# Kernel optimization log

Measured on AMD Instinct MI355X. Metric: run time of the kernel, lower is better.

Reference implementation:

```python
import jax, jax.numpy as jnp
import numpy as np

N_NODES = 100000
N_REL = 4
N_EDGES = 160000  # per relation
IN_F, HID_F, OUT_F = 128, 128, 64


def hetero_layer(x, edges, W, b):
    """Sum over relations of GraphConv (norm='both'): D_in^-1/2 A_r D_out^-1/2 X W_r + b_r."""
    N = x.shape[0]
    out = jnp.zeros((N, W.shape[2]), dtype=x.dtype)
    for r in range(W.shape[0]):  # small fixed relation count
        src = edges[r, 0]
        dst = edges[r, 1]
        ones = jnp.ones(src.shape[0], dtype=x.dtype)
        deg_out = jnp.clip(jax.ops.segment_sum(ones, src, num_segments=N), 1.0)
        deg_in = jnp.clip(jax.ops.segment_sum(ones, dst, num_segments=N), 1.0)
        # scale src features, project (W first since in_feats >= out_feats), gather, scatter-sum
        h = (x * jax.lax.rsqrt(deg_out)[:, None]) @ W[r]
        agg = jax.ops.segment_sum(h[src], dst, num_segments=N)
        out = out + agg * jax.lax.rsqrt(deg_in)[:, None] + b[r]
    return out


def setup_inputs() -> dict:
    key = jax.random.key(0)
    ks = jax.random.split(key, 6)
    x = jax.random.normal(ks[0], (N_NODES, IN_F), dtype=jnp.float32)
    edges = jax.random.randint(ks[1], (N_REL, 2, N_EDGES), 0, N_NODES, dtype=jnp.int32)
    W1 = jax.random.normal(ks[2], (N_REL, IN_F, HID_F), dtype=jnp.float32) * 0.05
    b1 = jnp.zeros((N_REL, HID_F), dtype=jnp.float32)
    W2 = jax.random.normal(ks[3], (N_REL, HID_F, OUT_F), dtype=jnp.float32) * 0.05
    b2 = jnp.zeros((N_REL, OUT_F), dtype=jnp.float32)
    return {"x": x, "edges": edges, "W1": W1, "b1": b1, "W2": W2, "b2": b2}


def reference(x, edges, W1, b1, W2, b2):
    h = jax.nn.relu(hetero_layer(x, edges, W1, b1))
    return hetero_layer(h, edges, W2, b2)
```

## Files before the change

kernel.cpp:

```cpp
#include <hip/hip_runtime.h>
#include <cstddef>
#include <cstdint>

#define NN   100000
#define NR   4
#define NE   160000
#define SCAN_B 1024
#define GEMMB 512

typedef short bf16x8 __attribute__((ext_vector_type(8)));
typedef float f32x4  __attribute__((ext_vector_type(4)));

__device__ __forceinline__ unsigned short f2bf(float f) {
  union { float f; unsigned u; } v; v.f = f;
  unsigned r = v.u + 0x7fffu + ((v.u >> 16) & 1u);
  return (unsigned short)(r >> 16);
}
__device__ __forceinline__ float bf2f(unsigned short h) {
  union { unsigned u; float f; } v; v.u = ((unsigned)h) << 16;
  return v.f;
}

__device__ __forceinline__ void gll16(const unsigned short* g, unsigned short* l) {
  __builtin_amdgcn_global_load_lds(
      (const __attribute__((address_space(1))) void*)g,
      (__attribute__((address_space(3))) void*)l, 16, 0, 0);
}

#define A_ZERO 782
#define A_NBLK (A_ZERO + 6250 + 256 + 128 + 1)
__global__ __launch_bounds__(256) void phaseA_k(const float* __restrict__ x,
                                                const float* __restrict__ W1,
                                                const float* __restrict__ W2,
                                                const float* __restrict__ b1,
                                                const float* __restrict__ b2,
                                                int* __restrict__ cnt,
                                                unsigned short* __restrict__ xb,
                                                unsigned short* __restrict__ Wt1,
                                                unsigned short* __restrict__ Wt2,
                                                float* __restrict__ bs1,
                                                float* __restrict__ bs2) {
  const int bid = blockIdx.x;
  const int t = threadIdx.x;
  if (bid < A_ZERO) {
    const int i = bid * 256 + t;
    if (i < 2 * NR * NN / 4) ((int4*)cnt)[i] = make_int4(0, 0, 0, 0);
  } else if (bid < A_ZERO + 6250) {
    const int i = (bid - A_ZERO) * 256 + t;
    const float4 a = *(const float4*)&x[(size_t)i * 8];
    const float4 b = *(const float4*)&x[(size_t)i * 8 + 4];
    unsigned short o[8];
    o[0] = f2bf(a.x); o[1] = f2bf(a.y); o[2] = f2bf(a.z); o[3] = f2bf(a.w);
    o[4] = f2bf(b.x); o[5] = f2bf(b.y); o[6] = f2bf(b.z); o[7] = f2bf(b.w);
    *(bf16x8*)&xb[(size_t)i * 8] = *(bf16x8*)o;
  } else if (bid < A_ZERO + 6250 + 256) {
    const int i = (bid - A_ZERO - 6250) * 256 + t;
    const int r = i / (128 * 128);
    const int k = (i / 128) % 128;
    const int n = i % 128;
    Wt1[((size_t)r * 128 + n) * 128 + k] = f2bf(W1[i]);
  } else if (bid < A_ZERO + 6250 + 256 + 128) {
    const int i = (bid - A_ZERO - 6250 - 256) * 256 + t;
    const int r = i / (128 * 64);
    const int k = (i / 64) % 128;
    const int n = i % 64;
    Wt2[((size_t)r * 64 + n) * 128 + k] = f2bf(W2[i]);
  } else {
    if (t < 128) bs1[t] = b1[t] + b1[128 + t] + b1[256 + t] + b1[384 + t];
    if (t < 64)  bs2[t] = b2[t] + b2[64 + t] + b2[128 + t] + b2[192 + t];
  }
}

template <int NOUT>
__device__ __forceinline__ void gemm_core(const unsigned short* __restrict__ Xb,
                                          const unsigned short* __restrict__ Wtr,
                                          unsigned short* __restrict__ Hr,
                                          int vb, unsigned short (*Xl)[64 * 128]) {
  const int t = threadIdx.x;
  const int wid = t >> 6;
  const int lane = t & 63;
  const int lg = lane >> 4;
  const int lr = lane & 15;

  constexpr int NF = (NOUT == 128) ? 4 : 2;
  const int rbase = (wid & 1) * 32;
  const int cbase = (wid >> 1) * (NOUT / 2);

  bf16x8 bw[NF][4];
#pragma unroll
  for (int nf = 0; nf < NF; ++nf)
#pragma unroll
    for (int ks = 0; ks < 4; ++ks)
      bw[nf][ks] = *(const bf16x8*)&Wtr[(size_t)(cbase + nf * 16 + lr) * 128 + ks * 32 + lg * 8];

  auto stage = [&](int buf, int tile) {
    const int row0 = tile * 64;
#pragma unroll
    for (int i = 0; i < 4; ++i) {
      const int rl = wid * 16 + i * 4 + (lane >> 4);
      int gr = row0 + rl;
      if (gr >= NN) gr = NN - 1;
      const int q = (lane & 15) ^ (rl & 7);
      gll16(&Xb[(size_t)gr * 128 + q * 8], &Xl[buf][rl * 128 + (lane & 15) * 8]);
    }
  };

  const int ntiles = (NN + 63) / 64;
  int tile = vb;
  stage(0, tile);
  __syncthreads();
  int buf = 0;

  for (; tile < ntiles; tile += 128) {
    const int nxt = tile + 128;
    if (nxt < ntiles) stage(buf ^ 1, nxt);

    f32x4 acc[2][NF];
#pragma unroll
    for (int mf = 0; mf < 2; ++mf)
#pragma unroll
      for (int nf = 0; nf < NF; ++nf) acc[mf][nf] = (f32x4){0.f, 0.f, 0.f, 0.f};

#pragma unroll
    for (int ks = 0; ks < 4; ++ks) {
#pragma unroll
      for (int mf = 0; mf < 2; ++mf) {
        const int r = rbase + mf * 16 + lr;
        const bf16x8 a =
            *(const bf16x8*)&Xl[buf][r * 128 + (((ks * 4 + lg) ^ (lr & 7)) << 3)];
#pragma unroll
        for (int nf = 0; nf < NF; ++nf)
          acc[mf][nf] = __builtin_amdgcn_mfma_f32_16x16x32_bf16(a, bw[nf][ks], acc[mf][nf], 0, 0, 0);
      }
    }

    const int row0 = tile * 64;
#pragma unroll
    for (int mf = 0; mf < 2; ++mf) {
#pragma unroll
      for (int i = 0; i < 4; ++i) {
        const int row = row0 + rbase + mf * 16 + lg * 4 + i;
        if (row < NN) {
#pragma unroll
          for (int nf = 0; nf < NF; ++nf)
            Hr[(size_t)row * NOUT + cbase + nf * 16 + lr] = f2bf(acc[mf][nf][i]);
        }
      }
    }
    __syncthreads();
    buf ^= 1;
  }
}

__global__ __launch_bounds__(256, 2) void phaseB_k(const int* __restrict__ edges,
                                                   const unsigned short* __restrict__ xb,
                                                   const unsigned short* __restrict__ Wt1,
                                                   unsigned short* __restrict__ H,
                                                   int* __restrict__ cnt_out,
                                                   int* __restrict__ cnt_in) {
  __shared__ unsigned short Xl[2][64 * 128];
  const int bid = blockIdx.x;
  if (bid < GEMMB) {
    const int z = bid >> 7;
    gemm_core<128>(xb, Wt1 + (size_t)z * 128 * 128, H + (size_t)z * NN * 128, bid & 127, Xl);
    return;
  }
  const int idx = bid - GEMMB;
  const int r = idx / 625;
  const int e = (idx - r * 625) * 256 + threadIdx.x;
  const int s = edges[(size_t)r * 2 * NE + e];
  const int d = edges[(size_t)r * 2 * NE + NE + e];
  atomicAdd(&cnt_out[(size_t)r * NN + s], 1);
  atomicAdd(&cnt_in[(size_t)r * NN + d], 1);
}

template <int NOUT>
__global__ __launch_bounds__(256, 2) void gemm3_k(const unsigned short* __restrict__ Xb,
                                                  const unsigned short* __restrict__ Wt,
                                                  unsigned short* __restrict__ H) {
  __shared__ unsigned short Xl[2][64 * 128];
  const int z = blockIdx.z;
  gemm_core<NOUT>(Xb, Wt + (size_t)z * NOUT * 128, H + (size_t)z * NN * NOUT, blockIdx.x, Xl);
}

__global__ __launch_bounds__(256) void scan1_k(const int* __restrict__ cnt_in,
                                               int* __restrict__ excl,
                                               int* __restrict__ bsum) {
  const int b = blockIdx.x, t = threadIdx.x;
  const int base = b * SCAN_B;
  int v[4]; int tl = 0;
#pragma unroll
  for (int i = 0; i < 4; ++i) {
    const int idx = base + t * 4 + i;
    int c = 0;
    if (idx < NN) {
      c = cnt_in[idx] + cnt_in[NN + idx] + cnt_in[2 * NN + idx] + cnt_in[3 * NN + idx];
    }
    v[i] = c;
    tl += c;
  }
  __shared__ int sm[256];
  sm[t] = tl;
  __syncthreads();
  for (int off = 1; off < 256; off <<= 1) {
    const int x = (t >= off) ? sm[t - off] : 0;
    __syncthreads();
    sm[t] += x;
    __syncthreads();
  }
  const int incl = sm[t];
  int run = incl - tl;
#pragma unroll
  for (int i = 0; i < 4; ++i) {
    const int idx = base + t * 4 + i;
    if (idx < NN) excl[idx] = run;
    run += v[i];
  }
  if (t == 255) bsum[b] = incl;
}

__global__ __launch_bounds__(128) void scan2_k(int* __restrict__ bsum, int nb) {
  const int t = threadIdx.x;
  __shared__ int sm[128];
  const int v = (t < nb) ? bsum[t] : 0;
  sm[t] = v;
  __syncthreads();
  for (int off = 1; off < 128; off <<= 1) {
    const int x = (t >= off) ? sm[t - off] : 0;
    __syncthreads();
    sm[t] += x;
    __syncthreads();
  }
  if (t < nb) bsum[t] = sm[t] - v;
}

__global__ __launch_bounds__(256) void scan3rs_k(const int* __restrict__ cnt,
                                                 float* __restrict__ rs,
                                                 const int* __restrict__ bsum,
                                                 int* __restrict__ row_ptr,
                                                 int* __restrict__ cursor) {
  const int bid = blockIdx.x, t = threadIdx.x;
  if (bid < 3125) {
    const int i = bid * 256 + t;
    rs[i] = rsqrtf(fmaxf((float)cnt[i], 1.0f));
  } else {
    const int i = (bid - 3125) * 256 + t;
    if (i < NN) {
      const int v = cursor[i] + bsum[i / SCAN_B];
      row_ptr[i] = v;
      cursor[i] = v;
    }
    if (i == 0) row_ptr[NN] = NR * NE;
  }
}

__global__ __launch_bounds__(256) void fill_k(const int* __restrict__ edges,
                                              const float* __restrict__ rs_out,
                                              const float* __restrict__ rs_in,
                                              int* __restrict__ cursor,
                                              int2* __restrict__ csr) {
  const int r = blockIdx.y;
  const int e = blockIdx.x * 256 + threadIdx.x;
  if (e >= NE) return;
  const int s = edges[(size_t)r * 2 * NE + e];
  const int d = edges[(size_t)r * 2 * NE + NE + e];
  const int pos = atomicAdd(&cursor[d], 1);
  const float w = rs_in[(size_t)r * NN + d] * rs_out[(size_t)r * NN + s];
  csr[pos] = make_int2(r * NN + s, __float_as_int(w));
}

__global__ __launch_bounds__(256) void gather1_k(const unsigned short* __restrict__ H,
                                                 const int* __restrict__ row_ptr,
                                                 const int2* __restrict__ csr,
                                                 const float* __restrict__ bs1,
                                                 unsigned short* __restrict__ h1b) {
  const int node = blockIdx.x * 4 + (threadIdx.x >> 6);
  const int lane = threadIdx.x & 63;
  if (node >= NN) return;
  const int g  = lane >> 4;
  const int fl = lane & 15;

  float acc[8];
#pragma unroll
  for (int j = 0; j < 8; ++j) acc[j] = 0.f;

  const int beg = row_ptr[node];
  const int end = row_ptr[node + 1];
  for (int e = beg + g; e < end; e += 4) {
    const int2 p = csr[e];
    const float w = __int_as_float(p.y);
    const bf16x8 h = *(const bf16x8*)&H[(size_t)p.x * 128 + fl * 8];
#pragma unroll
    for (int j = 0; j < 8; ++j)
      acc[j] = fmaf(bf2f((unsigned short)h[j]), w, acc[j]);
  }
#pragma unroll
  for (int j = 0; j < 8; ++j) {
    acc[j] += __shfl_xor(acc[j], 16);
    acc[j] += __shfl_xor(acc[j], 32);
  }
  if (g == 0) {
    const float4 c0 = *(const float4*)&bs1[fl * 8];
    const float4 c1 = *(const float4*)&bs1[fl * 8 + 4];
    unsigned short o[8];
    o[0] = f2bf(fmaxf(acc[0] + c0.x, 0.f));
    o[1] = f2bf(fmaxf(acc[1] + c0.y, 0.f));
    o[2] = f2bf(fmaxf(acc[2] + c0.z, 0.f));
    o[3] = f2bf(fmaxf(acc[3] + c0.w, 0.f));
    o[4] = f2bf(fmaxf(acc[4] + c1.x, 0.f));
    o[5] = f2bf(fmaxf(acc[5] + c1.y, 0.f));
    o[6] = f2bf(fmaxf(acc[6] + c1.z, 0.f));
    o[7] = f2bf(fmaxf(acc[7] + c1.w, 0.f));
    *(bf16x8*)&h1b[(size_t)node * 128 + fl * 8] = *(bf16x8*)o;
  }
}

__global__ __launch_bounds__(256) void gather2_k(const unsigned short* __restrict__ H,
                                                 const int* __restrict__ row_ptr,
                                                 const int2* __restrict__ csr,
                                                 const float* __restrict__ bs2,
                                                 float* __restrict__ out) {
  const int node = blockIdx.x * 4 + (threadIdx.x >> 6);
  const int lane = threadIdx.x & 63;
  if (node >= NN) return;
  const int g  = lane >> 3;
  const int fl = lane & 7;

  float acc[8];
#pragma unroll
  for (int j = 0; j < 8; ++j) acc[j] = 0.f;

  const int beg = row_ptr[node];
  const int end = row_ptr[node + 1];
  for (int e = beg + g; e < end; e += 8) {
    const int2 p = csr[e];
    const float w = __int_as_float(p.y);
    const bf16x8 h = *(const bf16x8*)&H[(size_t)p.x * 64 + fl * 8];
#pragma unroll
    for (int j = 0; j < 8; ++j)
      acc[j] = fmaf(bf2f((unsigned short)h[j]), w, acc[j]);
  }
#pragma unroll
  for (int j = 0; j < 8; ++j) {
    acc[j] += __shfl_xor(acc[j], 8);
    acc[j] += __shfl_xor(acc[j], 16);
    acc[j] += __shfl_xor(acc[j], 32);
  }
  if (g == 0) {
    const float4 c0 = *(const float4*)&bs2[fl * 8];
    const float4 c1 = *(const float4*)&bs2[fl * 8 + 4];
    float4 o0, o1;
    o0.x = acc[0] + c0.x; o0.y = acc[1] + c0.y; o0.z = acc[2] + c0.z; o0.w = acc[3] + c0.w;
    o1.x = acc[4] + c1.x; o1.y = acc[5] + c1.y; o1.z = acc[6] + c1.z; o1.w = acc[7] + c1.w;
    *(float4*)&out[(size_t)node * 64 + fl * 8]     = o0;
    *(float4*)&out[(size_t)node * 64 + fl * 8 + 4] = o1;
  }
}

extern "C" void kernel_launch(void* const* d_in, const int* in_sizes, int n_in,
                              void* d_out, int out_size, void* d_ws, size_t ws_size,
                              hipStream_t stream) {
  const float* x     = (const float*)d_in[0];
  const int*   edges = (const int*)d_in[1];
  const float* W1    = (const float*)d_in[2];
  const float* b1    = (const float*)d_in[3];
  const float* W2    = (const float*)d_in[4];
  const float* b2    = (const float*)d_in[5];
  float* out = (float*)d_out;

  unsigned short* xb   = (unsigned short*)d_ws;
  unsigned short* h1b  = xb;
  unsigned short* Hbuf = xb + (size_t)NN * 128;
  unsigned short* Wt1  = Hbuf + (size_t)NR * NN * 128;
  unsigned short* Wt2  = Wt1 + (size_t)NR * 128 * 128;
  float* rs_out = (float*)(Wt2 + (size_t)NR * 64 * 128);
  float* rs_in  = rs_out + (size_t)NR * NN;
  int* cnt_out  = (int*)(rs_in + (size_t)NR * NN);
  int* cnt_in   = cnt_out + (size_t)NR * NN;
  int* row_ptr  = cnt_in + (size_t)NR * NN;
  int* cursor   = row_ptr + (NN + 1);
  int* bsum     = cursor + NN;
  float* bs1    = (float*)(bsum + 128);
  float* bs2    = bs1 + 128;
  int2* csr     = (int2*)(bs2 + 64);

  const int nb = (NN + SCAN_B - 1) / SCAN_B;

  phaseA_k<<<A_NBLK, 256, 0, stream>>>(x, W1, W2, b1, b2, cnt_out, xb, Wt1, Wt2, bs1, bs2);
  phaseB_k<<<GEMMB + 2500, 256, 0, stream>>>(edges, xb, Wt1, Hbuf, cnt_out, cnt_in);
  scan1_k<<<nb, 256, 0, stream>>>(cnt_in, cursor , bsum);
  scan2_k<<<1, 128, 0, stream>>>(bsum, nb);
  scan3rs_k<<<3125 + (NN + 255) / 256, 256, 0, stream>>>(cnt_out, rs_out, bsum, row_ptr, cursor);
  fill_k<<<dim3((NE + 255) / 256, NR), 256, 0, stream>>>(edges, rs_out, rs_in, cursor, csr);
  gather1_k<<<(NN + 3) / 4, 256, 0, stream>>>(Hbuf, row_ptr, csr, bs1, h1b);
  gemm3_k<64><<<dim3(128, 1, NR), 256, 0, stream>>>(h1b, Wt2, Hbuf);
  gather2_k<<<(NN + 3) / 4, 256, 0, stream>>>(Hbuf, row_ptr, csr, bs2, out);
}
```

Before: 214.9 us.

## Share staged X tiles across two relations per GEMM block; memset counters

Each GEMM block now computes two relations from the same staged X tile in LDS. This halves the number of times each node-feature row is loaded from global memory, for both the first-layer and second-layer projections. The counter zeroing moves out of the conversion kernel into hipMemsetAsync. The cost is doubled accumulator and weight register use per thread, which can lower occupancy or cause spills under launch_bounds(256,2), and half as many GEMM blocks are launched.

```diff
diff --git a/kernel.cpp b/kernel.cpp
--- a/kernel.cpp
+++ b/kernel.cpp
@@ -6,7 +6,7 @@
 #define NR   4
 #define NE   160000
 #define SCAN_B 1024
-#define GEMMB 512
+#define GEMMB1 256
 
 typedef short bf16x8 __attribute__((ext_vector_type(8)));
 typedef float f32x4  __attribute__((ext_vector_type(4)));
@@ -27,40 +27,35 @@
       (__attribute__((address_space(3))) void*)l, 16, 0, 0);
 }
 
-#define A_ZERO 782
-#define A_NBLK (A_ZERO + 6250 + 256 + 128 + 1)
-__global__ __launch_bounds__(256) void phaseA_k(const float* __restrict__ x,
-                                                const float* __restrict__ W1,
-                                                const float* __restrict__ W2,
-                                                const float* __restrict__ b1,
-                                                const float* __restrict__ b2,
-                                                int* __restrict__ cnt,
-                                                unsigned short* __restrict__ xb,
-                                                unsigned short* __restrict__ Wt1,
-                                                unsigned short* __restrict__ Wt2,
-                                                float* __restrict__ bs1,
-                                                float* __restrict__ bs2) {
+#define CVT_NBLK 6635
+__global__ __launch_bounds__(256) void cvtA_k(const float* __restrict__ x,
+                                              const float* __restrict__ W1,
+                                              const float* __restrict__ W2,
+                                              const float* __restrict__ b1,
+                                              const float* __restrict__ b2,
+                                              unsigned short* __restrict__ xb,
+                                              unsigned short* __restrict__ Wt1,
+                                              unsigned short* __restrict__ Wt2,
+                                              float* __restrict__ bs1,
+                                              float* __restrict__ bs2) {
   const int bid = blockIdx.x;
   const int t = threadIdx.x;
-  if (bid < A_ZERO) {
+  if (bid < 6250) {
     const int i = bid * 256 + t;
-    if (i < 2 * NR * NN / 4) ((int4*)cnt)[i] = make_int4(0, 0, 0, 0);
-  } else if (bid < A_ZERO + 6250) {
-    const int i = (bid - A_ZERO) * 256 + t;
     const float4 a = *(const float4*)&x[(size_t)i * 8];
     const float4 b = *(const float4*)&x[(size_t)i * 8 + 4];
     unsigned short o[8];
     o[0] = f2bf(a.x); o[1] = f2bf(a.y); o[2] = f2bf(a.z); o[3] = f2bf(a.w);
     o[4] = f2bf(b.x); o[5] = f2bf(b.y); o[6] = f2bf(b.z); o[7] = f2bf(b.w);
     *(bf16x8*)&xb[(size_t)i * 8] = *(bf16x8*)o;
-  } else if (bid < A_ZERO + 6250 + 256) {
-    const int i = (bid - A_ZERO - 6250) * 256 + t;
+  } else if (bid < 6506) {
+    const int i = (bid - 6250) * 256 + t;
     const int r = i / (128 * 128);
     const int k = (i / 128) % 128;
     const int n = i % 128;
     Wt1[((size_t)r * 128 + n) * 128 + k] = f2bf(W1[i]);
-  } else if (bid < A_ZERO + 6250 + 256 + 128) {
-    const int i = (bid - A_ZERO - 6250 - 256) * 256 + t;
+  } else if (bid < 6634) {
+    const int i = (bid - 6506) * 256 + t;
     const int r = i / (128 * 64);
     const int k = (i / 64) % 128;
     const int n = i % 64;
@@ -72,26 +67,30 @@
 }
 
 template <int NOUT>
-__device__ __forceinline__ void gemm_core(const unsigned short* __restrict__ Xb,
-                                          const unsigned short* __restrict__ Wtr,
-                                          unsigned short* __restrict__ Hr,
-                                          int vb, unsigned short (*Xl)[64 * 128]) {
+__device__ __forceinline__ void gemm_dual_core(const unsigned short* __restrict__ Xb,
+                                               const unsigned short* __restrict__ W0,
+                                               const unsigned short* __restrict__ W1,
+                                               unsigned short* __restrict__ H0,
+                                               unsigned short* __restrict__ H1,
+                                               int vb, unsigned short (*Xl)[64 * 128]) {
   const int t = threadIdx.x;
   const int wid = t >> 6;
   const int lane = t & 63;
   const int lg = lane >> 4;
   const int lr = lane & 15;
 
-  constexpr int NF = (NOUT == 128) ? 4 : 2;
+  constexpr int NF = NOUT / 32;
   const int rbase = (wid & 1) * 32;
   const int cbase = (wid >> 1) * (NOUT / 2);
 
-  bf16x8 bw[NF][4];
+  bf16x8 bw[2][NF][4];
 #pragma unroll
   for (int nf = 0; nf < NF; ++nf)
 #pragma unroll
-    for (int ks = 0; ks < 4; ++ks)
-      bw[nf][ks] = *(const bf16x8*)&Wtr[(size_t)(cbase + nf * 16 + lr) * 128 + ks * 32 + lg * 8];
+    for (int ks = 0; ks < 4; ++ks) {
+      bw[0][nf][ks] = *(const bf16x8*)&W0[(size_t)(cbase + nf * 16 + lr) * 128 + ks * 32 + lg * 8];
+      bw[1][nf][ks] = *(const bf16x8*)&W1[(size_t)(cbase + nf * 16 + lr) * 128 + ks * 32 + lg * 8];
+    }
 
   auto stage = [&](int buf, int tile) {
     const int row0 = tile * 64;
@@ -115,11 +114,13 @@
     const int nxt = tile + 128;
     if (nxt < ntiles) stage(buf ^ 1, nxt);
 
-    f32x4 acc[2][NF];
+    f32x4 acc[2][2][NF];
 #pragma unroll
     for (int mf = 0; mf < 2; ++mf)
 #pragma unroll
-      for (int nf = 0; nf < NF; ++nf) acc[mf][nf] = (f32x4){0.f, 0.f, 0.f, 0.f};
+      for (int rel = 0; rel < 2; ++rel)
+#pragma unroll
+        for (int nf = 0; nf < NF; ++nf) acc[mf][rel][nf] = (f32x4){0.f, 0.f, 0.f, 0.f};
 
 #pragma unroll
     for (int ks = 0; ks < 4; ++ks) {
@@ -129,8 +130,10 @@
         const bf16x8 a =
             *(const bf16x8*)&Xl[buf][r * 128 + (((ks * 4 + lg) ^ (lr & 7)) << 3)];
 #pragma unroll
-        for (int nf = 0; nf < NF; ++nf)
-          acc[mf][nf] = __builtin_amdgcn_mfma_f32_16x16x32_bf16(a, bw[nf][ks], acc[mf][nf], 0, 0, 0);
+        for (int rel = 0; rel < 2; ++rel)
+#pragma unroll
+          for (int nf = 0; nf < NF; ++nf)
+            acc[mf][rel][nf] = __builtin_amdgcn_mfma_f32_16x16x32_bf16(a, bw[rel][nf][ks], acc[mf][rel][nf], 0, 0, 0);
       }
     }
 
@@ -142,8 +145,10 @@
         const int row = row0 + rbase + mf * 16 + lg * 4 + i;
         if (row < NN) {
 #pragma unroll
-          for (int nf = 0; nf < NF; ++nf)
-            Hr[(size_t)row * NOUT + cbase + nf * 16 + lr] = f2bf(acc[mf][nf][i]);
+          for (int nf = 0; nf < NF; ++nf) {
+            H0[(size_t)row * NOUT + cbase + nf * 16 + lr] = f2bf(acc[mf][0][nf][i]);
+            H1[(size_t)row * NOUT + cbase + nf * 16 + lr] = f2bf(acc[mf][1][nf][i]);
+          }
         }
       }
     }
@@ -160,12 +165,17 @@
                                                    int* __restrict__ cnt_in) {
   __shared__ unsigned short Xl[2][64 * 128];
   const int bid = blockIdx.x;
-  if (bid < GEMMB) {
-    const int z = bid >> 7;
-    gemm_core<128>(xb, Wt1 + (size_t)z * 128 * 128, H + (size_t)z * NN * 128, bid & 127, Xl);
+  if (bid < GEMMB1) {
+    const int zp = bid >> 7;
+    gemm_dual_core<128>(xb,
+                        Wt1 + (size_t)(2 * zp) * 128 * 128,
+                        Wt1 + (size_t)(2 * zp + 1) * 128 * 128,
+                        H + (size_t)(2 * zp) * NN * 128,
+                        H + (size_t)(2 * zp + 1) * NN * 128,
+                        bid & 127, Xl);
     return;
   }
-  const int idx = bid - GEMMB;
+  const int idx = bid - GEMMB1;
   const int r = idx / 625;
   const int e = (idx - r * 625) * 256 + threadIdx.x;
   const int s = edges[(size_t)r * 2 * NE + e];
@@ -174,13 +184,17 @@
   atomicAdd(&cnt_in[(size_t)r * NN + d], 1);
 }
 
-template <int NOUT>
-__global__ __launch_bounds__(256, 2) void gemm3_k(const unsigned short* __restrict__ Xb,
-                                                  const unsigned short* __restrict__ Wt,
-                                                  unsigned short* __restrict__ H) {
+__global__ __launch_bounds__(256, 2) void gemm_dual_k(const unsigned short* __restrict__ Xb,
+                                                      const unsigned short* __restrict__ Wt,
+                                                      unsigned short* __restrict__ H) {
   __shared__ unsigned short Xl[2][64 * 128];
-  const int z = blockIdx.z;
-  gemm_core<NOUT>(Xb, Wt + (size_t)z * NOUT * 128, H + (size_t)z * NN * NOUT, blockIdx.x, Xl);
+  const int zp = blockIdx.z;
+  gemm_dual_core<64>(Xb,
+                     Wt + (size_t)(2 * zp) * 64 * 128,
+                     Wt + (size_t)(2 * zp + 1) * 64 * 128,
+                     H + (size_t)(2 * zp) * NN * 64,
+                     H + (size_t)(2 * zp + 1) * NN * 64,
+                     blockIdx.x, Xl);
 }
 
 __global__ __launch_bounds__(256) void scan1_k(const int* __restrict__ cnt_in,
@@ -386,13 +400,14 @@
 
   const int nb = (NN + SCAN_B - 1) / SCAN_B;
 
-  phaseA_k<<<A_NBLK, 256, 0, stream>>>(x, W1, W2, b1, b2, cnt_out, xb, Wt1, Wt2, bs1, bs2);
-  phaseB_k<<<GEMMB + 2500, 256, 0, stream>>>(edges, xb, Wt1, Hbuf, cnt_out, cnt_in);
+  hipMemsetAsync(cnt_out, 0, (size_t)2 * NR * NN * sizeof(int), stream);
+  cvtA_k<<<CVT_NBLK, 256, 0, stream>>>(x, W1, W2, b1, b2, xb, Wt1, Wt2, bs1, bs2);
+  phaseB_k<<<GEMMB1 + 2500, 256, 0, stream>>>(edges, xb, Wt1, Hbuf, cnt_out, cnt_in);
   scan1_k<<<nb, 256, 0, stream>>>(cnt_in, cursor , bsum);
   scan2_k<<<1, 128, 0, stream>>>(bsum, nb);
   scan3rs_k<<<3125 + (NN + 255) / 256, 256, 0, stream>>>(cnt_out, rs_out, bsum, row_ptr, cursor);
   fill_k<<<dim3((NE + 255) / 256, NR), 256, 0, stream>>>(edges, rs_out, rs_in, cursor, csr);
   gather1_k<<<(NN + 3) / 4, 256, 0, stream>>>(Hbuf, row_ptr, csr, bs1, h1b);
-  gemm3_k<64><<<dim3(128, 1, NR), 256, 0, stream>>>(h1b, Wt2, Hbuf);
+  gemm_dual_k<<<dim3(128, 1, 2), 256, 0, stream>>>(h1b, Wt2, Hbuf);
   gather2_k<<<(NN + 3) / 4, 256, 0, stream>>>(Hbuf, row_ptr, csr, bs2, out);
 }
```

Result: slower. 281.1 us (+30.8%).
